# Optimization experiments

Measured on AMD Instinct MI355X. Metric: run time of the kernel, lower is better.

The kernel has to match this reference:

```python
import jax, jax.numpy as jnp
import numpy as np

B, C, H, W = 8, 512, 64, 128
K = 19          # num_classes
BH, BW = 2, 4   # bin_size
N = BH * BW     # bin_num
CI = C // 2     # feat_inner


def setup_inputs() -> dict:
    ks = jax.random.split(jax.random.key(0), 10)
    def nrm(k, shape, s=0.02):
        return jax.random.normal(k, shape, jnp.float32) * s
    return {
        "x": jax.random.normal(ks[0], (B, C, H, W), jnp.float32),
        "conv_cam_w": nrm(ks[1], (K, C)),
        "conv_cam_b": jnp.zeros((K,), jnp.float32),
        "gcn_w1": nrm(ks[2], (N, N), 0.1),
        "gcn_a": jnp.full((N,), 0.25, jnp.float32),
        "gcn_w2": nrm(ks[3], (C, C)),
        "fuse_w": nrm(ks[4], (1, N), 0.1),
        "fuse_b": jnp.zeros((1,), jnp.float32),
        "relu_a": jnp.full((1,), 0.25, jnp.float32),
        "q_w": nrm(ks[5], (CI, C)),
        "q_b": jnp.zeros((CI,), jnp.float32),
        "k_w": nrm(ks[6], (CI, C)),
        "k_b": jnp.zeros((CI,), jnp.float32),
        "v_w": nrm(ks[7], (CI, C)),
        "v_b": jnp.zeros((CI,), jnp.float32),
        "out_w": nrm(ks[8], (C, CI)),
        "bn_gamma": jnp.ones((C,), jnp.float32),
        "bn_beta": jnp.zeros((C,), jnp.float32),
        "out_a": jnp.full((C,), 0.25, jnp.float32),
    }


def _prelu(x, a):
    return jnp.maximum(x, 0) + a * jnp.minimum(x, 0)


def _split(t):
    # [b, cc, H, W] -> [b, N, rh*rw, cc]  (patch_split)
    b, cc = t.shape[0], t.shape[1]
    rh, rw = H // BH, W // BW
    t = t.reshape(b, cc, BH, rh, BW, rw).transpose(0, 2, 4, 3, 5, 1)
    return t.reshape(b, N, rh * rw, cc)


def _caam(x, conv_cam_w, conv_cam_b, gcn_w1, gcn_a, gcn_w2, fuse_w, fuse_b,
          relu_a, q_w, q_b, k_w, k_b, v_w, v_b, out_w, bn_gamma, bn_beta, out_a):
    b = x.shape[0]
    rh, rw = H // BH, W // BW
    # CAM (1x1 conv) + adaptive avg pool to bins + sigmoid
    cam = jnp.einsum('bchw,kc->bkhw', x, conv_cam_w) + conv_cam_b[None, :, None, None]
    cls_score = jax.nn.sigmoid(cam.reshape(b, K, BH, rh, BW, rw).mean((3, 5)))  # [b,K,BH,BW]
    cam_p = _split(cam)   # [b,N,P,K]
    x_p = _split(x)       # [b,N,P,C]
    bin_conf = cls_score.reshape(b, K, N).transpose(0, 2, 1)[..., None]  # [b,N,K,1]
    pix_conf = jax.nn.softmax(cam_p, axis=2)
    local = jnp.einsum('bnpk,bnpc->bnkc', pix_conf, x_p) * bin_conf  # [b,N,K,C]
    # GCN: conv1 over bin dim, PReLU(residual), Linear over channels
    t = jnp.einsum('nm,bmkc->bnkc', gcn_w1, local)
    t = _prelu(t + local, gcn_a[None, :, None, None])
    local = jnp.einsum('bnkc,dc->bnkd', t, gcn_w2)
    # fuse bins -> single global descriptor, PReLU(1)
    glob = jnp.einsum('on,bnkc->bokc', fuse_w, local) + fuse_b[None, :, None, None]  # [b,1,K,C]
    glob = _prelu(glob[:, 0], relu_a[0])  # [b,K,C]
    # QKV attention over bins (key/value over K class slots)
    q = jnp.einsum('bnpc,ic->bnpi', x_p, q_w) + q_b       # [b,N,P,CI]
    key = jnp.einsum('bnkc,ic->bnki', local, k_w) + k_b   # [b,N,K,CI]
    val = jnp.einsum('bkc,ic->bki', glob, v_w) + v_b      # [b,K,CI] (shared across bins)
    aff = jax.nn.softmax(jnp.einsum('bnpi,bnki->bnpk', q, key), axis=-1)
    out = jnp.einsum('bnpk,bki->bnpi', aff, val)          # [b,N,P,CI]
    # patch_recover -> [b,CI,H,W]
    out = out.reshape(b, BH, BW, rh, rw, CI).transpose(0, 5, 1, 3, 2, 4).reshape(b, CI, H, W)
    # conv_out: 1x1 conv (no bias) + BatchNorm2d (batch stats) + PReLU(C)
    y = jnp.einsum('bihw,ci->bchw', out, out_w)
    mu = y.mean((0, 2, 3), keepdims=True)
    var = y.var((0, 2, 3), keepdims=True)
    y = (y - mu) * jax.lax.rsqrt(var + 1e-5)
    y = y * bn_gamma[None, :, None, None] + bn_beta[None, :, None, None]
    y = _prelu(y, out_a[None, :, None, None])
    return x + y


def reference(x, conv_cam_w, conv_cam_b, gcn_w1, gcn_a, gcn_w2, fuse_w, fuse_b,
              relu_a, q_w, q_b, k_w, k_b, v_w, v_b, out_w, bn_gamma, bn_beta, out_a):
    return _caam(x, conv_cam_w, conv_cam_b, gcn_w1, gcn_a, gcn_w2, fuse_w, fuse_b,
                 relu_a, q_w, q_b, k_w, k_b, v_w, v_b, out_w, bn_gamma, bn_beta, out_a)
```

## Files before the change

### kernel.cpp

```cpp
#include <hip/hip_runtime.h>
#include <cstdint>
#include <cstddef>

#define B_ 8
#define C_ 512
#define H_ 64
#define W_ 128
#define HW_ 8192
#define K_ 19
#define N_ 8
#define P_ 1024
#define CI_ 256

typedef unsigned short u16;
typedef unsigned int u32;
typedef __attribute__((ext_vector_type(8))) short bf16x8;
typedef __attribute__((ext_vector_type(4))) float f32x4;

__device__ __forceinline__ u16 f2bf(float f) {
  u32 u = __float_as_uint(f);
  u32 r = (u + 0x7FFFu + ((u >> 16) & 1u)) >> 16;
  return (u16)r;
}
__device__ __forceinline__ float bf2f(u16 h) {
  return __uint_as_float(((u32)h) << 16);
}

__device__ __forceinline__ void gload16(const u16* g, u16* l) {
  __builtin_amdgcn_global_load_lds(
      (const __attribute__((address_space(1))) unsigned int*)g,
      (__attribute__((address_space(3))) unsigned int*)l, 16, 0, 0);
}

__device__ __forceinline__ void stage128(const u16* __restrict__ src, size_t ld, int k0,
                                         u16* lds, int wave, int lane) {
  int rsub = lane >> 3;
  int swz = ((lane & 7) ^ rsub) << 3;
#pragma unroll
  for (int i = 0; i < 4; i++) {
    int rowbase = wave * 8 + i * 32;
    gload16(src + (size_t)(rowbase + rsub) * ld + k0 + swz, lds + rowbase * 64);
  }
}
__device__ __forceinline__ void stage32(const u16* __restrict__ src, size_t ld, int k0,
                                        u16* lds, int wave, int lane) {
  int rsub = lane >> 3;
  int swz = ((lane & 7) ^ rsub) << 3;
  int rowbase = wave * 8;
  gload16(src + (size_t)(rowbase + rsub) * ld + k0 + swz, lds + rowbase * 64);
}
__device__ __forceinline__ bf16x8 frag(const u16* lds, int row, int qbyte) {
  return *(const bf16x8*)((const char*)lds + row * 128 + (qbyte ^ ((row & 7) << 4)));
}

__device__ __forceinline__ float blockSum256(float v, float* red4) {
#pragma unroll
  for (int o = 32; o > 0; o >>= 1) v += __shfl_down(v, o, 64);
  __syncthreads();
  if ((threadIdx.x & 63) == 0) red4[threadIdx.x >> 6] = v;
  __syncthreads();
  return red4[0] + red4[1] + red4[2] + red4[3];
}

__device__ __forceinline__ float blockMax256(float v, float* red4) {
#pragma unroll
  for (int o = 32; o > 0; o >>= 1) v = fmaxf(v, __shfl_down(v, o, 64));
  __syncthreads();
  if ((threadIdx.x & 63) == 0) red4[threadIdx.x >> 6] = v;
  __syncthreads();
  return fmaxf(fmaxf(red4[0], red4[1]), fmaxf(red4[2], red4[3]));
}

__device__ __forceinline__ void cvt4(const float* __restrict__ s, u16* __restrict__ d, int i) {
  float4 v = *(const float4*)&s[(size_t)i * 4];
  ushort4 o;
  o.x = f2bf(v.x); o.y = f2bf(v.y); o.z = f2bf(v.z); o.w = f2bf(v.w);
  *(ushort4*)&d[(size_t)i * 4] = o;
}

__global__ __launch_bounds__(256) void xpose_prep_kernel(const float* __restrict__ x,
                                                         u16* __restrict__ xt,
                                                         const float* __restrict__ qw,
                                                         const float* __restrict__ ow,
                                                         const float* __restrict__ kw,
                                                         const float* __restrict__ gw2,
                                                         const float* __restrict__ camw,
                                                         u16* __restrict__ qwbf,
                                                         u16* __restrict__ owbf,
                                                         u16* __restrict__ kwbf,
                                                         u16* __restrict__ gw2bf,
                                                         u16* __restrict__ camwbf,
                                                         float* __restrict__ sums,
                                                         float* __restrict__ tpad) {
  __shared__ float tile[64][65];
  int bid = blockIdx.x;
  int tid = threadIdx.x;
  if (bid >= 8192) {
    int pb = bid - 8192;
    if (pb < 128) {
      cvt4(qw, qwbf, pb * 256 + tid);
    } else if (pb < 256) {
      cvt4(ow, owbf, (pb - 128) * 256 + tid);
    } else if (pb < 384) {
      cvt4(kw, kwbf, (pb - 256) * 256 + tid);
    } else if (pb < 640) {
      cvt4(gw2, gw2bf, (pb - 384) * 256 + tid);
    } else if (pb < 656) {
      int i = (pb - 640) * 256 + tid;
      if (i * 4 < K_ * C_) {
        cvt4(camw, camwbf, i);
      } else {
        ushort4 z; z.x = 0; z.y = 0; z.z = 0; z.w = 0;
        *(ushort4*)&camwbf[(size_t)i * 4] = z;
      }
    } else if (pb == 656) {
      float4 z; z.x = 0.f; z.y = 0.f; z.z = 0.f; z.w = 0.f;
      *(float4*)&sums[tid * 4] = z;
    } else {
      int i = (pb - 657) * 256 + tid;
      float4 z; z.x = 0.f; z.y = 0.f; z.z = 0.f; z.w = 0.f;
      *(float4*)&tpad[(size_t)i * 4] = z;
    }
    return;
  }
  int hw0 = (bid & 127) << 6;
  int c0 = ((bid >> 7) & 7) << 6;
  int b = bid >> 10;
  int r = tid >> 4;
  int col4 = (tid & 15) << 2;
  const float* xb = x + ((size_t)b * C_ + c0) * HW_ + hw0;
#pragma unroll
  for (int it = 0; it < 4; it++) {
    int rr = r + it * 16;
    float4 v = *(const float4*)&xb[(size_t)rr * HW_ + col4];
    tile[rr][col4 + 0] = v.x;
    tile[rr][col4 + 1] = v.y;
    tile[rr][col4 + 2] = v.z;
    tile[rr][col4 + 3] = v.w;
  }
  __syncthreads();
  u16* xo = xt + ((size_t)b * HW_ + hw0) * C_ + c0;
#pragma unroll
  for (int it = 0; it < 4; it++) {
    int hwr = r + it * 16;
    ushort4 o;
    o.x = f2bf(tile[col4 + 0][hwr]);
    o.y = f2bf(tile[col4 + 1][hwr]);
    o.z = f2bf(tile[col4 + 2][hwr]);
    o.w = f2bf(tile[col4 + 3][hwr]);
    *(ushort4*)&xo[(size_t)hwr * C_ + col4] = o;
  }
}

__global__ __launch_bounds__(256) void gemm_cam_kernel(const u16* __restrict__ A,
                                                       const u16* __restrict__ Bw,
                                                       const float* __restrict__ bias,
                                                       float* __restrict__ cam) {
  __shared__ __align__(16) u16 As[128 * 64];
  __shared__ __align__(16) u16 Bs[32 * 64];
  int b = blockIdx.y;
  int m0 = blockIdx.x * 128;
  int tid = threadIdx.x;
  int wave = tid >> 6, lane = tid & 63;
  int wm = wave * 32;
  int quad = lane >> 4, l16 = lane & 15;
  const u16* Ab = A + (size_t)b * HW_ * C_ + (size_t)m0 * C_;
  f32x4 acc[2][2] = {};
  for (int k0 = 0; k0 < C_; k0 += 64) {
    __syncthreads();
    stage128(Ab, C_, k0, As, wave, lane);
    stage32(Bw, C_, k0, Bs, wave, lane);
    __syncthreads();
#pragma unroll
    for (int kk = 0; kk < 2; kk++) {
      int qb_ = kk * 64 + quad * 16;
      bf16x8 af[2], bfv[2];
#pragma unroll
      for (int t = 0; t < 2; t++) {
        af[t] = frag(As, wm + t * 16 + l16, qb_);
        bfv[t] = frag(Bs, t * 16 + l16, qb_);
      }
#pragma unroll
      for (int tm = 0; tm < 2; tm++)
#pragma unroll
        for (int tn = 0; tn < 2; tn++)
          acc[tm][tn] = __builtin_amdgcn_mfma_f32_16x16x32_bf16(af[tm], bfv[tn], acc[tm][tn], 0, 0, 0);
    }
  }
  float* C = cam + (size_t)b * K_ * HW_;
#pragma unroll
  for (int tm = 0; tm < 2; tm++) {
    int mm = m0 + wm + tm * 16 + quad * 4;
#pragma unroll
    for (int tn = 0; tn < 2; tn++) {
      int nn = tn * 16 + l16;
      if (nn < K_) {
        float bv = bias[nn];
        f32x4 v = acc[tm][tn];
        v[0] += bv; v[1] += bv; v[2] += bv; v[3] += bv;
        *(f32x4*)&C[(size_t)nn * HW_ + mm] = v;
      }
    }
  }
}

__global__ __launch_bounds__(256) void softcls_kernel(const float* __restrict__ cam,
                                                      float* __restrict__ bconf,
                                                      float* __restrict__ pconf) {
  __shared__ float red4[4];
  int bid = blockIdx.x;
  int k = bid % 19;
  int n = (bid / 19) & 7;
  int b = bid / 152;
  int bh = n >> 2, bw = n & 3;
  const float* base = cam + ((size_t)b * K_ + k) * HW_ + (bh * 32) * W_ + bw * 32;
  float v[4];
  float s = 0.f, mx = -1e30f;
#pragma unroll
  for (int j = 0; j < 4; j++) {
    int p = threadIdx.x + j * 256;
    v[j] = base[(p >> 5) * W_ + (p & 31)];
    s += v[j];
    mx = fmaxf(mx, v[j]);
  }
  float tot = blockSum256(s, red4);
  if (threadIdx.x == 0) {
    float m = tot * (1.f / 1024.f);
    bconf[bid] = 1.f / (1.f + __expf(-m));
  }
  mx = blockMax256(mx, red4);
  float e[4];
  float se = 0.f;
#pragma unroll
  for (int j = 0; j < 4; j++) { e[j] = __expf(v[j] - mx); se += e[j]; }
  se = blockSum256(se, red4);
  float inv = 1.f / se;
  float* outp = pconf + (size_t)bid * P_;
#pragma unroll
  for (int j = 0; j < 4; j++) outp[threadIdx.x + j * 256] = e[j] * inv;
}

__global__ __launch_bounds__(256) void local_part_kernel(const u16* __restrict__ xt,
                                                         const float* __restrict__ pconf,
                                                         float* __restrict__ part) {
  __shared__ __align__(16) float pcl[19 * 256];
  int bid = blockIdx.x;
  int pq = bid & 3;
  int half = (bid >> 2) & 1;
  int n = (bid >> 3) & 7;
  int b = bid >> 6;
  int tid = threadIdx.x;
  int c = half * 256 + tid;
  int bh = n >> 2, bw = n & 3;
  const float* pcb = pconf + (size_t)((b * N_ + n) * K_) * P_ + pq * 256;
  for (int e = tid; e < 19 * 64; e += 256) {
    int k = e >> 6, q4 = e & 63;
    *(float4*)&pcl[k * 256 + q4 * 4] = *(const float4*)&pcb[(size_t)k * P_ + q4 * 4];
  }
  __syncthreads();
  float acc[K_];
#pragma unroll
  for (int k = 0; k < K_; k++) acc[k] = 0.f;
  const u16* xb = xt + (size_t)b * HW_ * C_ + c;
  for (int pl0 = 0; pl0 < 256; pl0 += 8) {
    float xv[8];
#pragma unroll
    for (int g = 0; g < 2; g++) {
      int p = pq * 256 + pl0 + g * 4;
      int hw = (bh * 32 + (p >> 5)) * W_ + bw * 32 + (p & 31);
      const u16* xr = xb + (size_t)hw * C_;
#pragma unroll
      for (int j = 0; j < 4; j++) xv[g * 4 + j] = bf2f(xr[(size_t)j * C_]);
    }
#pragma unroll
    for (int k = 0; k < K_; k++) {
      float4 p0 = *(const float4*)&pcl[k * 256 + pl0];
      float4 p1 = *(const float4*)&pcl[k * 256 + pl0 + 4];
      acc[k] += p0.x * xv[0] + p0.y * xv[1] + p0.z * xv[2] + p0.w * xv[3]
              + p1.x * xv[4] + p1.y * xv[5] + p1.z * xv[6] + p1.w * xv[7];
    }
  }
  int row = (b * N_ + n) * K_;
  float* pp = part + ((size_t)pq * 1216 + row) * C_ + c;
#pragma unroll
  for (int k = 0; k < K_; k++) pp[(size_t)k * C_] = acc[k];
}

__global__ __launch_bounds__(256) void t_kernel(const float* __restrict__ part,
                                                const float* __restrict__ bconf,
                                                const float* __restrict__ gw1,
                                                const float* __restrict__ ga,
                                                u16* __restrict__ tbuf) {
  __shared__ float gw1l[64];
  __shared__ float gal[8];
  __shared__ float bcl[8];
  int tid = threadIdx.x;
  int bid = blockIdx.x;
  int half = bid & 1;
  int rem = bid >> 1;
  int k = rem % 19;
  int b = rem / 19;
  if (tid < 64) gw1l[tid] = gw1[tid];
  if (tid < 8) {
    gal[tid] = ga[tid];
    bcl[tid] = bconf[(size_t)(b * 8 + tid) * 19 + k];
  }
  __syncthreads();
  int c = half * 256 + tid;
  float lm[8];
#pragma unroll
  for (int m = 0; m < 8; m++) {
    size_t off = ((size_t)(b * N_ + m) * K_ + k) * C_ + c;
    lm[m] = (part[off] + part[off + (size_t)1216 * 512] +
             part[off + (size_t)2 * 1216 * 512] + part[off + (size_t)3 * 1216 * 512]) * bcl[m];
  }
#pragma unroll
  for (int n = 0; n < 8; n++) {
    float v = lm[n];
#pragma unroll
    for (int m = 0; m < 8; m++) v += gw1l[n * 8 + m] * lm[m];
    float t = fmaxf(v, 0.f) + gal[n] * fminf(v, 0.f);
    tbuf[((size_t)((b * N_ + n) * K_ + k)) * C_ + c] = f2bf(t);
  }
}

template <int KDIM, int NDIM, bool BIAS>
__device__ __forceinline__ void gemm_small_body(int bidx,
                                                const u16* __restrict__ A,
                                                const u16* __restrict__ Bw,
                                                const float* __restrict__ bias,
                                                float* __restrict__ f32out,
                                                u16* __restrict__ bf16out,
                                                u16* As, u16* Bs) {
  constexpr int NT = NDIM / 128;
  int m0 = (bidx / NT) * 128;
  int n0 = (bidx % NT) * 128;
  int tid = threadIdx.x;
  int wave = tid >> 6, lane = tid & 63;
  int wm = (wave >> 1) * 64, wn = (wave & 1) * 64;
  int quad = lane >> 4, l16 = lane & 15;
  const u16* Ab = A + (size_t)m0 * KDIM;
  const u16* Bb = Bw + (size_t)n0 * KDIM;
  f32x4 acc[4][4] = {};
  for (int k0 = 0; k0 < KDIM; k0 += 64) {
    __syncthreads();
    stage128(Ab, KDIM, k0, As, wave, lane);
    stage128(Bb, KDIM, k0, Bs, wave, lane);
    __syncthreads();
#pragma unroll
    for (int kk = 0; kk < 2; kk++) {
      int qb_ = kk * 64 + quad * 16;
      bf16x8 af[4], bfv[4];
#pragma unroll
      for (int t = 0; t < 4; t++) {
        af[t] = frag(As, wm + t * 16 + l16, qb_);
        bfv[t] = frag(Bs, wn + t * 16 + l16, qb_);
      }
#pragma unroll
      for (int tm = 0; tm < 4; tm++)
#pragma unroll
        for (int tn = 0; tn < 4; tn++)
          acc[tm][tn] = __builtin_amdgcn_mfma_f32_16x16x32_bf16(af[tm], bfv[tn], acc[tm][tn], 0, 0, 0);
    }
  }
  float bv[4];
#pragma unroll
  for (int tn = 0; tn < 4; tn++)
    bv[tn] = BIAS ? bias[n0 + wn + tn * 16 + l16] : 0.f;
#pragma unroll
  for (int tm = 0; tm < 4; tm++) {
    int mm = m0 + wm + tm * 16 + quad * 4;
#pragma unroll
    for (int tn = 0; tn < 4; tn++) {
      int nn = n0 + wn + tn * 16 + l16;
#pragma unroll
      for (int reg = 0; reg < 4; reg++) {
        float v = acc[tm][tn][reg] + bv[tn];
        if (f32out) f32out[(size_t)(mm + reg) * NDIM + nn] = v;
        if (bf16out) bf16out[(size_t)(mm + reg) * NDIM + nn] = f2bf(v);
      }
    }
  }
}

template <int KDIM, int NDIM, bool BIAS>
__global__ __launch_bounds__(256) void gemm_small_kernel(const u16* __restrict__ A,
                                                         const u16* __restrict__ Bw,
                                                         const float* __restrict__ bias,
                                                         float* __restrict__ f32out,
                                                         u16* __restrict__ bf16out) {
  __shared__ __align__(16) u16 As[128 * 64];
  __shared__ __align__(16) u16 Bs[128 * 64];
  gemm_small_body<KDIM, NDIM, BIAS>(blockIdx.x, A, Bw, bias, f32out, bf16out, As, Bs);
}

__device__ __forceinline__ void glob_val_body(int bid,
                                              const float* __restrict__ locl2,
                                              const float* __restrict__ fw,
                                              const float* __restrict__ fb,
                                              const float* __restrict__ ra,
                                              const float* __restrict__ vw,
                                              const float* __restrict__ vb,
                                              float* __restrict__ valo,
                                              float* gl) {
  int k = bid % 19;
  int b = bid / 19;
  int tid = threadIdx.x;
  float fwr[8];
#pragma unroll
  for (int m = 0; m < 8; m++) fwr[m] = fw[m];
  float fbv = fb[0], rav = ra[0];
  const float* lb = locl2 + ((size_t)(b * N_) * K_ + k) * C_;
  for (int c = tid; c < C_; c += 256) {
    float v = fbv;
#pragma unroll
    for (int m = 0; m < 8; m++) v += fwr[m] * lb[(size_t)m * K_ * C_ + c];
    gl[c] = fmaxf(v, 0.f) + rav * fminf(v, 0.f);
  }
  __syncthreads();
  int i = tid;
  const float* wr = vw + (size_t)i * C_;
  float s = vb[i];
  for (int c4 = 0; c4 < C_; c4 += 4) {
    float4 wv = *(const float4*)&wr[c4];
    float4 tv = *(const float4*)&gl[c4];
    s += wv.x * tv.x + wv.y * tv.y + wv.z * tv.z + wv.w * tv.w;
  }
  valo[(size_t)bid * CI_ + i] = s;
}

__global__ __launch_bounds__(256) void small2_globval_kernel(const u16* __restrict__ A,
                                                             const u16* __restrict__ Bw,
                                                             const float* __restrict__ bias,
                                                             float* __restrict__ keyo,
                                                             const float* __restrict__ locl2,
                                                             const float* __restrict__ fw,
                                                             const float* __restrict__ fb,
                                                             const float* __restrict__ ra,
                                                             const float* __restrict__ vw,
                                                             const float* __restrict__ vb,
                                                             float* __restrict__ valo) {
  __shared__ __align__(16) u16 As[128 * 64];
  __shared__ __align__(16) u16 Bs[128 * 64];
  if (blockIdx.x < 20) {
    gemm_small_body<512, 256, true>(blockIdx.x, A, Bw, bias, keyo, nullptr, As, Bs);
  } else {
    glob_val_body(blockIdx.x - 20, locl2, fw, fb, ra, vw, vb, valo, (float*)As);
  }
}

template <int KDIM, int NDIM, bool TRANS_OUT, bool BIAS, bool OUTBF16, bool BNSTAT>
__global__ __launch_bounds__(256) void gemm_big_kernel(const u16* __restrict__ A,
                                                       const u16* __restrict__ Bw,
                                                       const float* __restrict__ bias,
                                                       void* __restrict__ Cout,
                                                       float* __restrict__ sums,
                                                       float* __restrict__ sumsq) {
  __shared__ __align__(16) u16 As[128 * 64];
  __shared__ __align__(16) u16 Bs[128 * 64];
  constexpr int NT = NDIM / 128;
  int b = blockIdx.y;
  int d = blockIdx.x;
  int xcd = d & 7;
  int j = d >> 3;
  int m0 = (xcd + 8 * (j / NT)) * 128;
  int n0 = (j % NT) * 128;
  int tid = threadIdx.x;
  int wave = tid >> 6, lane = tid & 63;
  int wm = (wave >> 1) * 64, wn = (wave & 1) * 64;
  int quad = lane >> 4, l16 = lane & 15;
  const u16* Ab = A + (size_t)b * 8192 * KDIM + (size_t)m0 * KDIM;
  const u16* Bb = Bw + (size_t)n0 * KDIM;
  f32x4 acc[4][4] = {};
  for (int k0 = 0; k0 < KDIM; k0 += 64) {
    __syncthreads();
    stage128(Ab, KDIM, k0, As, wave, lane);
    stage128(Bb, KDIM, k0, Bs, wave, lane);
    __syncthreads();
#pragma unroll
    for (int kk = 0; kk < 2; kk++) {
      int qb_ = kk * 64 + quad * 16;
      bf16x8 af[4], bfv[4];
#pragma unroll
      for (int t = 0; t < 4; t++) {
        af[t] = frag(As, wm + t * 16 + l16, qb_);
        bfv[t] = frag(Bs, wn + t * 16 + l16, qb_);
      }
#pragma unroll
      for (int tm = 0; tm < 4; tm++)
#pragma unroll
        for (int tn = 0; tn < 4; tn++)
          acc[tm][tn] = __builtin_amdgcn_mfma_f32_16x16x32_bf16(af[tm], bfv[tn], acc[tm][tn], 0, 0, 0);
    }
  }
  if constexpr (!TRANS_OUT) {
    float bv[4];
#pragma unroll
    for (int tn = 0; tn < 4; tn++)
      bv[tn] = BIAS ? bias[n0 + wn + tn * 16 + l16] : 0.f;
#pragma unroll
    for (int tm = 0; tm < 4; tm++) {
      int mm = m0 + wm + tm * 16 + quad * 4;
#pragma unroll
      for (int tn = 0; tn < 4; tn++) {
        int nn = n0 + wn + tn * 16 + l16;
        if constexpr (OUTBF16) {
          u16* C = (u16*)Cout + (size_t)b * 8192 * NDIM;
#pragma unroll
          for (int reg = 0; reg < 4; reg++)
            C[(size_t)(mm + reg) * NDIM + nn] = f2bf(acc[tm][tn][reg] + bv[tn]);
        } else {
          float* C = (float*)Cout + (size_t)b * 8192 * NDIM;
#pragma unroll
          for (int reg = 0; reg < 4; reg++)
            C[(size_t)(mm + reg) * NDIM + nn] = acc[tm][tn][reg] + bv[tn];
        }
      }
    }
  } else {
    float* C = (float*)Cout + (size_t)b * NDIM * 8192;
#pragma unroll
    for (int tm = 0; tm < 4; tm++) {
      int mm = m0 + wm + tm * 16 + quad * 4;
#pragma unroll
      for (int tn = 0; tn < 4; tn++) {
        int nn = n0 + wn + tn * 16 + l16;
        *(f32x4*)&C[(size_t)nn * 8192 + mm] = acc[tm][tn];
      }
    }
    if constexpr (BNSTAT) {
#pragma unroll
      for (int tn = 0; tn < 4; tn++) {
        int nn = n0 + wn + tn * 16 + l16;
        float s = 0.f, q = 0.f;
#pragma unroll
        for (int tm = 0; tm < 4; tm++)
#pragma unroll
          for (int reg = 0; reg < 4; reg++) {
            float v = acc[tm][tn][reg];
            s += v;
            q += v * v;
          }
        s += __shfl_xor(s, 16, 64); q += __shfl_xor(q, 16, 64);
        s += __shfl_xor(s, 32, 64); q += __shfl_xor(q, 32, 64);
        if (quad == 0) {
          atomicAdd(&sums[nn], s);
          atomicAdd(&sumsq[nn], q);
        }
      }
    }
  }
}

__global__ __launch_bounds__(256) void attn2_kernel(const u16* __restrict__ q,
                                                    const float* __restrict__ keyo,
                                                    const float* __restrict__ valo,
                                                    u16* __restrict__ obuf) {
  __shared__ float keyl[19 * 256];
  __shared__ float vall[19 * 256];
  __shared__ float aff[128 * 20];
  int bid = blockIdx.x;
  int rg = bid & 7;
  int n = (bid >> 3) & 7;
  int b = bid >> 6;
  int bh = n >> 2, bw = n & 3;
  int tid = threadIdx.x;
  const float* ksrc = keyo + (size_t)((b * 8 + n) * 19) * 256;
  for (int e = tid; e < 19 * 256; e += 256) keyl[e] = ksrc[e];
  __syncthreads();
  if (tid < 128) {
    int r = rg * 4 + (tid >> 5);
    int wc = tid & 31;
    int hw = (bh * 32 + r) * W_ + bw * 32 + wc;
    const u16* qr = q + ((size_t)b * HW_ + hw) * 256;
    float acc[19];
#pragma unroll
    for (int k = 0; k < 19; k++) acc[k] = 0.f;
    for (int i0 = 0; i0 < 256; i0 += 8) {
      uint4 v = *(const uint4*)&qr[i0];
      float f0 = __uint_as_float((v.x & 0xFFFFu) << 16);
      float f1 = __uint_as_float(v.x & 0xFFFF0000u);
      float f2 = __uint_as_float((v.y & 0xFFFFu) << 16);
      float f3 = __uint_as_float(v.y & 0xFFFF0000u);
      float f4 = __uint_as_float((v.z & 0xFFFFu) << 16);
      float f5 = __uint_as_float(v.z & 0xFFFF0000u);
      float f6 = __uint_as_float((v.w & 0xFFFFu) << 16);
      float f7 = __uint_as_float(v.w & 0xFFFF0000u);
#pragma unroll
      for (int k = 0; k < 19; k++) {
        const float* kr = &keyl[k * 256 + i0];
        acc[k] += f0 * kr[0] + f1 * kr[1] + f2 * kr[2] + f3 * kr[3] +
                  f4 * kr[4] + f5 * kr[5] + f6 * kr[6] + f7 * kr[7];
      }
    }
    float mx = -1e30f;
#pragma unroll
    for (int k = 0; k < 19; k++) mx = fmaxf(mx, acc[k]);
    float se = 0.f;
#pragma unroll
    for (int k = 0; k < 19; k++) { acc[k] = __expf(acc[k] - mx); se += acc[k]; }
    float inv = 1.f / se;
#pragma unroll
    for (int k = 0; k < 19; k++) aff[tid * 20 + k] = acc[k] * inv;
  } else {
    const float* vsrc = valo + (size_t)b * 19 * 256;
    for (int e = tid - 128; e < 19 * 256; e += 128) vall[e] = vsrc[e];
  }
  __syncthreads();
  int px = tid & 127;
  int ih = (tid >> 7) * 128;
  int r3 = rg * 4 + (px >> 5);
  int wc3 = px & 31;
  int hw3 = (bh * 32 + r3) * W_ + bw * 32 + wc3;
  float av[19];
#pragma unroll
  for (int k = 0; k < 19; k++) av[k] = aff[px * 20 + k];
  u16* ob = obuf + ((size_t)b * HW_ + hw3) * 256 + ih;
  for (int i0 = 0; i0 < 128; i0 += 16) {
    float o16[16];
#pragma unroll
    for (int j = 0; j < 16; j++) o16[j] = 0.f;
#pragma unroll
    for (int k = 0; k < 19; k++) {
      float a = av[k];
      const float* vr = &vall[k * 256 + ih + i0];
#pragma unroll
      for (int j = 0; j < 16; j++) o16[j] += a * vr[j];
    }
    uint4 w0, w1;
    w0.x = (u32)f2bf(o16[0]) | ((u32)f2bf(o16[1]) << 16);
    w0.y = (u32)f2bf(o16[2]) | ((u32)f2bf(o16[3]) << 16);
    w0.z = (u32)f2bf(o16[4]) | ((u32)f2bf(o16[5]) << 16);
    w0.w = (u32)f2bf(o16[6]) | ((u32)f2bf(o16[7]) << 16);
    w1.x = (u32)f2bf(o16[8]) | ((u32)f2bf(o16[9]) << 16);
    w1.y = (u32)f2bf(o16[10]) | ((u32)f2bf(o16[11]) << 16);
    w1.z = (u32)f2bf(o16[12]) | ((u32)f2bf(o16[13]) << 16);
    w1.w = (u32)f2bf(o16[14]) | ((u32)f2bf(o16[15]) << 16);
    *(uint4*)&ob[i0] = w0;
    *(uint4*)&ob[i0 + 8] = w1;
  }
}

__global__ __launch_bounds__(256) void final_kernel(const float* __restrict__ x,
                                                    const float* __restrict__ sums,
                                                    const float* __restrict__ sumsq,
                                                    const float* __restrict__ gamma,
                                                    const float* __restrict__ beta,
                                                    const float* __restrict__ oa,
                                                    float* __restrict__ out) {
  size_t base = (size_t)blockIdx.x * 4096 + threadIdx.x * 4;
  int c = (int)((base >> 13) & 511);
  const float inv_cnt = 1.f / 65536.f;
  float mu = sums[c] * inv_cnt;
  float var = sumsq[c] * inv_cnt - mu * mu;
  float iv = rsqrtf(var + 1e-5f);
  float sc = gamma[c] * iv;
  float sh = beta[c] - mu * sc;
  float a = oa[c];
#pragma unroll
  for (int jj = 0; jj < 4; jj++) {
    size_t idx = base + (size_t)jj * 1024;
    float4 y = *(float4*)&out[idx];
    float4 xv = *(const float4*)&x[idx];
    float4 r;
    float t;
    t = y.x * sc + sh; r.x = xv.x + fmaxf(t, 0.f) + a * fminf(t, 0.f);
    t = y.y * sc + sh; r.y = xv.y + fmaxf(t, 0.f) + a * fminf(t, 0.f);
    t = y.z * sc + sh; r.z = xv.z + fmaxf(t, 0.f) + a * fminf(t, 0.f);
    t = y.w * sc + sh; r.w = xv.w + fmaxf(t, 0.f) + a * fminf(t, 0.f);
    *(float4*)&out[idx] = r;
  }
}

extern "C" void kernel_launch(void* const* d_in, const int* in_sizes, int n_in,
                              void* d_out, int out_size, void* d_ws, size_t ws_size,
                              hipStream_t stream) {
  const float* x     = (const float*)d_in[0];
  const float* camw  = (const float*)d_in[1];
  const float* camb  = (const float*)d_in[2];
  const float* gw1   = (const float*)d_in[3];
  const float* ga    = (const float*)d_in[4];
  const float* gw2   = (const float*)d_in[5];
  const float* fw    = (const float*)d_in[6];
  const float* fb    = (const float*)d_in[7];
  const float* ra    = (const float*)d_in[8];
  const float* qw    = (const float*)d_in[9];
  const float* qb    = (const float*)d_in[10];
  const float* kw    = (const float*)d_in[11];
  const float* kb    = (const float*)d_in[12];
  const float* vw    = (const float*)d_in[13];
  const float* vb    = (const float*)d_in[14];
  const float* ow    = (const float*)d_in[15];
  const float* gamma = (const float*)d_in[16];
  const float* beta  = (const float*)d_in[17];
  const float* oa    = (const float*)d_in[18];
  float* out = (float*)d_out;
  float* ws = (float*)d_ws;

  float* cam    = ws;
  float* bconf  = cam + 1245184;
  float* pconf  = bconf + 2048;
  float* locl   = pconf + 1245184;
  float* locl2f = locl + 622592;
  float* keyo   = locl2f + 655360;
  float* valo   = keyo + 327680;
  float* sums   = valo + 38912;
  float* sumsq  = sums + 512;
  float* scale  = sumsq + 512;
  float* shift  = scale + 512;
  u16* qwbf   = (u16*)(shift + 512);
  u16* owbf   = qwbf + 131072;
  u16* kwbf   = owbf + 131072;
  u16* gw2bf  = kwbf + 131072;
  u16* camwbf = gw2bf + 262144;
  u16* tbuf   = camwbf + 16384;
  u16* l2bf   = tbuf + 655360;
  u16* xt     = l2bf + 655360;
  u16* obuf   = xt;
  u16* qbuf   = xt + 33554432;
  float* part = (float*)qbuf;

  xpose_prep_kernel<<<8865, 256, 0, stream>>>(x, xt, qw, ow, kw, gw2, camw,
                                              qwbf, owbf, kwbf, gw2bf, camwbf,
                                              sums, (float*)(tbuf + 1216 * 512));
  gemm_cam_kernel<<<dim3(64, 8), 256, 0, stream>>>(xt, camwbf, camb, cam);
  softcls_kernel<<<1216, 256, 0, stream>>>(cam, bconf, pconf);
  local_part_kernel<<<512, 256, 0, stream>>>(xt, pconf, part);
  t_kernel<<<304, 256, 0, stream>>>(part, bconf, gw1, ga, tbuf);
  gemm_small_kernel<512, 512, false>
      <<<40, 256, 0, stream>>>(tbuf, gw2bf, nullptr, locl2f, l2bf);
  small2_globval_kernel<<<172, 256, 0, stream>>>(l2bf, kwbf, kb, keyo,
                                                 locl2f, fw, fb, ra, vw, vb, valo);
  gemm_big_kernel<512, 256, false, true, true, false>
      <<<dim3(128, 8), 256, 0, stream>>>(xt, qwbf, qb, qbuf, nullptr, nullptr);
  attn2_kernel<<<512, 256, 0, stream>>>(qbuf, keyo, valo, obuf);
  gemm_big_kernel<256, 512, true, false, false, true>
      <<<dim3(256, 8), 256, 0, stream>>>(obuf, owbf, nullptr, out, sums, sumsq);
  final_kernel<<<8192, 256, 0, stream>>>(x, sums, sumsq, gamma, beta, oa, out);
}
```

Before: 549.3 us.

## Fold query and output projections into low-rank key/value products

Reassociates the attention: each bin's keys are pre-multiplied by the query weights (qw^T·key, giving a 512x19 matrix per bin plus a bias term). The values are pre-multiplied by the output conv weights, giving a 19x512 matrix per batch. Affinities then come from a thin GEMM of x against 19 columns, and the output is rebuilt as aff·vo inside the final kernel, with BN statistics computed from the affinities. This removes the two big 8192x512x256 GEMMs and the bf16 intermediate q/o buffers. The cost is recomputing y in a scalar loop in the final kernel with strided per-channel stores, plus a small serial weight-fold kernel.

```diff
diff --git a/kernel.cpp b/kernel.cpp
--- a/kernel.cpp
+++ b/kernel.cpp
@@ -80,13 +80,9 @@
 
 __global__ __launch_bounds__(256) void xpose_prep_kernel(const float* __restrict__ x,
                                                          u16* __restrict__ xt,
-                                                         const float* __restrict__ qw,
-                                                         const float* __restrict__ ow,
                                                          const float* __restrict__ kw,
                                                          const float* __restrict__ gw2,
                                                          const float* __restrict__ camw,
-                                                         u16* __restrict__ qwbf,
-                                                         u16* __restrict__ owbf,
                                                          u16* __restrict__ kwbf,
                                                          u16* __restrict__ gw2bf,
                                                          u16* __restrict__ camwbf,
@@ -98,26 +94,22 @@
   if (bid >= 8192) {
     int pb = bid - 8192;
     if (pb < 128) {
-      cvt4(qw, qwbf, pb * 256 + tid);
-    } else if (pb < 256) {
-      cvt4(ow, owbf, (pb - 128) * 256 + tid);
+      cvt4(kw, kwbf, pb * 256 + tid);
     } else if (pb < 384) {
-      cvt4(kw, kwbf, (pb - 256) * 256 + tid);
-    } else if (pb < 640) {
-      cvt4(gw2, gw2bf, (pb - 384) * 256 + tid);
-    } else if (pb < 656) {
-      int i = (pb - 640) * 256 + tid;
+      cvt4(gw2, gw2bf, (pb - 128) * 256 + tid);
+    } else if (pb < 400) {
+      int i = (pb - 384) * 256 + tid;
       if (i * 4 < K_ * C_) {
         cvt4(camw, camwbf, i);
       } else {
         ushort4 z; z.x = 0; z.y = 0; z.z = 0; z.w = 0;
         *(ushort4*)&camwbf[(size_t)i * 4] = z;
       }
-    } else if (pb == 656) {
+    } else if (pb == 400) {
       float4 z; z.x = 0.f; z.y = 0.f; z.z = 0.f; z.w = 0.f;
       *(float4*)&sums[tid * 4] = z;
     } else {
-      int i = (pb - 657) * 256 + tid;
+      int i = (pb - 401) * 256 + tid;
       float4 z; z.x = 0.f; z.y = 0.f; z.z = 0.f; z.w = 0.f;
       *(float4*)&tpad[(size_t)i * 4] = z;
     }
@@ -449,226 +441,217 @@
   }
 }
 
-template <int KDIM, int NDIM, bool TRANS_OUT, bool BIAS, bool OUTBF16, bool BNSTAT>
-__global__ __launch_bounds__(256) void gemm_big_kernel(const u16* __restrict__ A,
-                                                       const u16* __restrict__ Bw,
-                                                       const float* __restrict__ bias,
-                                                       void* __restrict__ Cout,
-                                                       float* __restrict__ sums,
-                                                       float* __restrict__ sumsq) {
+__global__ __launch_bounds__(256) void qk2vo_kernel(const float* __restrict__ keyo,
+                                                    const float* __restrict__ qw,
+                                                    const float* __restrict__ qb,
+                                                    const float* __restrict__ valo,
+                                                    const float* __restrict__ ow,
+                                                    u16* __restrict__ qk2bf,
+                                                    float* __restrict__ sbias,
+                                                    float* __restrict__ vo) {
+  __shared__ float kl[19 * 256];
+  int bid = blockIdx.x, tid = threadIdx.x;
+  if (bid < 64) {
+    const float* ks = keyo + (size_t)bid * 19 * 256;
+    for (int e = tid; e < 19 * 256; e += 256) kl[e] = ks[e];
+    __syncthreads();
+    if (tid < 19) {
+      float s = 0.f;
+      for (int i = 0; i < 256; i++) s += qb[i] * kl[tid * 256 + i];
+      sbias[(size_t)bid * 19 + tid] = s;
+    }
+    float a0[19], a1[19];
+#pragma unroll
+    for (int k = 0; k < 19; k++) { a0[k] = 0.f; a1[k] = 0.f; }
+    for (int i = 0; i < 256; i++) {
+      float q0 = qw[(size_t)i * 512 + tid];
+      float q1 = qw[(size_t)i * 512 + 256 + tid];
+#pragma unroll
+      for (int k = 0; k < 19; k++) {
+        float kv = kl[k * 256 + i];
+        a0[k] += q0 * kv;
+        a1[k] += q1 * kv;
+      }
+    }
+    u16* qo = qk2bf + (size_t)bid * 32 * 512;
+#pragma unroll
+    for (int k = 0; k < 19; k++) {
+      qo[k * 512 + tid] = f2bf(a0[k]);
+      qo[k * 512 + 256 + tid] = f2bf(a1[k]);
+    }
+  } else {
+    int b = bid - 64;
+    const float* vs = valo + (size_t)b * 19 * 256;
+    for (int e = tid; e < 19 * 256; e += 256) kl[e] = vs[e];
+    __syncthreads();
+    float a0[19], a1[19];
+#pragma unroll
+    for (int k = 0; k < 19; k++) { a0[k] = 0.f; a1[k] = 0.f; }
+    for (int i = 0; i < 256; i++) {
+      float w0 = ow[(size_t)tid * 256 + i];
+      float w1 = ow[(size_t)(tid + 256) * 256 + i];
+#pragma unroll
+      for (int k = 0; k < 19; k++) {
+        float kv = kl[k * 256 + i];
+        a0[k] += w0 * kv;
+        a1[k] += w1 * kv;
+      }
+    }
+    float* vob = vo + (size_t)b * 19 * 512;
+#pragma unroll
+    for (int k = 0; k < 19; k++) {
+      vob[k * 512 + tid] = a0[k];
+      vob[k * 512 + 256 + tid] = a1[k];
+    }
+  }
+}
+
+__global__ __launch_bounds__(256) void attn3_kernel(const u16* __restrict__ xt,
+                                                    const u16* __restrict__ qk2bf,
+                                                    const float* __restrict__ sbias,
+                                                    const float* __restrict__ vo,
+                                                    float* __restrict__ aff,
+                                                    float* __restrict__ sums,
+                                                    float* __restrict__ sumsq) {
   __shared__ __align__(16) u16 As[128 * 64];
-  __shared__ __align__(16) u16 Bs[128 * 64];
-  constexpr int NT = NDIM / 128;
-  int b = blockIdx.y;
-  int d = blockIdx.x;
-  int xcd = d & 7;
-  int j = d >> 3;
-  int m0 = (xcd + 8 * (j / NT)) * 128;
-  int n0 = (j % NT) * 128;
+  __shared__ __align__(16) u16 Bs[32 * 64];
+  __shared__ __align__(16) float aff_l[128][24];
+  int bid = blockIdx.x;
+  int mt = bid & 7, n = (bid >> 3) & 7, b = bid >> 6;
+  int bh = n >> 2, bw = n & 3;
   int tid = threadIdx.x;
   int wave = tid >> 6, lane = tid & 63;
-  int wm = (wave >> 1) * 64, wn = (wave & 1) * 64;
+  int wm = wave * 32;
   int quad = lane >> 4, l16 = lane & 15;
-  const u16* Ab = A + (size_t)b * 8192 * KDIM + (size_t)m0 * KDIM;
-  const u16* Bb = Bw + (size_t)n0 * KDIM;
-  f32x4 acc[4][4] = {};
-  for (int k0 = 0; k0 < KDIM; k0 += 64) {
+  int hwbase = bh * 4096 + bw * 32 + mt * 512;
+  const u16* Ab = xt + ((size_t)b * HW_ + hwbase) * C_;
+  const u16* Bb = qk2bf + (size_t)(b * 8 + n) * 32 * 512;
+  f32x4 acc[2][2] = {};
+  int rsub = lane >> 3;
+  int swz = ((lane & 7) ^ rsub) << 3;
+  for (int k0 = 0; k0 < C_; k0 += 64) {
     __syncthreads();
-    stage128(Ab, KDIM, k0, As, wave, lane);
-    stage128(Bb, KDIM, k0, Bs, wave, lane);
+#pragma unroll
+    for (int i = 0; i < 4; i++) {
+      int rb = wave * 8 + i * 32;
+      int r = rb + rsub;
+      gload16(Ab + (size_t)((r >> 5) * 128 + (r & 31)) * C_ + k0 + swz, As + rb * 64);
+    }
+    stage32(Bb, 512, k0, Bs, wave, lane);
     __syncthreads();
 #pragma unroll
     for (int kk = 0; kk < 2; kk++) {
       int qb_ = kk * 64 + quad * 16;
-      bf16x8 af[4], bfv[4];
-#pragma unroll
-      for (int t = 0; t < 4; t++) {
-        af[t] = frag(As, wm + t * 16 + l16, qb_);
-        bfv[t] = frag(Bs, wn + t * 16 + l16, qb_);
+      bf16x8 af2[2], bfv[2];
+#pragma unroll
+      for (int t = 0; t < 2; t++) {
+        af2[t] = frag(As, wm + t * 16 + l16, qb_);
+        bfv[t] = frag(Bs, t * 16 + l16, qb_);
       }
 #pragma unroll
-      for (int tm = 0; tm < 4; tm++)
-#pragma unroll
-        for (int tn = 0; tn < 4; tn++)
-          acc[tm][tn] = __builtin_amdgcn_mfma_f32_16x16x32_bf16(af[tm], bfv[tn], acc[tm][tn], 0, 0, 0);
-    }
-  }
-  if constexpr (!TRANS_OUT) {
-    float bv[4];
-#pragma unroll
-    for (int tn = 0; tn < 4; tn++)
-      bv[tn] = BIAS ? bias[n0 + wn + tn * 16 + l16] : 0.f;
-#pragma unroll
-    for (int tm = 0; tm < 4; tm++) {
-      int mm = m0 + wm + tm * 16 + quad * 4;
-#pragma unroll
-      for (int tn = 0; tn < 4; tn++) {
-        int nn = n0 + wn + tn * 16 + l16;
-        if constexpr (OUTBF16) {
-          u16* C = (u16*)Cout + (size_t)b * 8192 * NDIM;
-#pragma unroll
-          for (int reg = 0; reg < 4; reg++)
-            C[(size_t)(mm + reg) * NDIM + nn] = f2bf(acc[tm][tn][reg] + bv[tn]);
-        } else {
-          float* C = (float*)Cout + (size_t)b * 8192 * NDIM;
-#pragma unroll
-          for (int reg = 0; reg < 4; reg++)
-            C[(size_t)(mm + reg) * NDIM + nn] = acc[tm][tn][reg] + bv[tn];
-        }
-      }
-    }
-  } else {
-    float* C = (float*)Cout + (size_t)b * NDIM * 8192;
-#pragma unroll
-    for (int tm = 0; tm < 4; tm++) {
-      int mm = m0 + wm + tm * 16 + quad * 4;
-#pragma unroll
-      for (int tn = 0; tn < 4; tn++) {
-        int nn = n0 + wn + tn * 16 + l16;
-        *(f32x4*)&C[(size_t)nn * 8192 + mm] = acc[tm][tn];
-      }
-    }
-    if constexpr (BNSTAT) {
-#pragma unroll
-      for (int tn = 0; tn < 4; tn++) {
-        int nn = n0 + wn + tn * 16 + l16;
-        float s = 0.f, q = 0.f;
-#pragma unroll
-        for (int tm = 0; tm < 4; tm++)
-#pragma unroll
-          for (int reg = 0; reg < 4; reg++) {
-            float v = acc[tm][tn][reg];
-            s += v;
-            q += v * v;
-          }
-        s += __shfl_xor(s, 16, 64); q += __shfl_xor(q, 16, 64);
-        s += __shfl_xor(s, 32, 64); q += __shfl_xor(q, 32, 64);
-        if (quad == 0) {
-          atomicAdd(&sums[nn], s);
-          atomicAdd(&sumsq[nn], q);
-        }
-      }
-    }
-  }
-}
-
-__global__ __launch_bounds__(256) void attn2_kernel(const u16* __restrict__ q,
-                                                    const float* __restrict__ keyo,
-                                                    const float* __restrict__ valo,
-                                                    u16* __restrict__ obuf) {
-  __shared__ float keyl[19 * 256];
-  __shared__ float vall[19 * 256];
-  __shared__ float aff[128 * 20];
-  int bid = blockIdx.x;
-  int rg = bid & 7;
-  int n = (bid >> 3) & 7;
-  int b = bid >> 6;
-  int bh = n >> 2, bw = n & 3;
-  int tid = threadIdx.x;
-  const float* ksrc = keyo + (size_t)((b * 8 + n) * 19) * 256;
-  for (int e = tid; e < 19 * 256; e += 256) keyl[e] = ksrc[e];
-  __syncthreads();
-  if (tid < 128) {
-    int r = rg * 4 + (tid >> 5);
-    int wc = tid & 31;
-    int hw = (bh * 32 + r) * W_ + bw * 32 + wc;
-    const u16* qr = q + ((size_t)b * HW_ + hw) * 256;
-    float acc[19];
-#pragma unroll
-    for (int k = 0; k < 19; k++) acc[k] = 0.f;
-    for (int i0 = 0; i0 < 256; i0 += 8) {
-      uint4 v = *(const uint4*)&qr[i0];
-      float f0 = __uint_as_float((v.x & 0xFFFFu) << 16);
-      float f1 = __uint_as_float(v.x & 0xFFFF0000u);
-      float f2 = __uint_as_float((v.y & 0xFFFFu) << 16);
-      float f3 = __uint_as_float(v.y & 0xFFFF0000u);
-      float f4 = __uint_as_float((v.z & 0xFFFFu) << 16);
-      float f5 = __uint_as_float(v.z & 0xFFFF0000u);
-      float f6 = __uint_as_float((v.w & 0xFFFFu) << 16);
-      float f7 = __uint_as_float(v.w & 0xFFFF0000u);
-#pragma unroll
-      for (int k = 0; k < 19; k++) {
-        const float* kr = &keyl[k * 256 + i0];
-        acc[k] += f0 * kr[0] + f1 * kr[1] + f2 * kr[2] + f3 * kr[3] +
-                  f4 * kr[4] + f5 * kr[5] + f6 * kr[6] + f7 * kr[7];
-      }
-    }
-    float mx = -1e30f;
-#pragma unroll
-    for (int k = 0; k < 19; k++) mx = fmaxf(mx, acc[k]);
-    float se = 0.f;
-#pragma unroll
-    for (int k = 0; k < 19; k++) { acc[k] = __expf(acc[k] - mx); se += acc[k]; }
-    float inv = 1.f / se;
-#pragma unroll
-    for (int k = 0; k < 19; k++) aff[tid * 20 + k] = acc[k] * inv;
-  } else {
-    const float* vsrc = valo + (size_t)b * 19 * 256;
-    for (int e = tid - 128; e < 19 * 256; e += 128) vall[e] = vsrc[e];
-  }
-  __syncthreads();
-  int px = tid & 127;
-  int ih = (tid >> 7) * 128;
-  int r3 = rg * 4 + (px >> 5);
-  int wc3 = px & 31;
-  int hw3 = (bh * 32 + r3) * W_ + bw * 32 + wc3;
-  float av[19];
-#pragma unroll
-  for (int k = 0; k < 19; k++) av[k] = aff[px * 20 + k];
-  u16* ob = obuf + ((size_t)b * HW_ + hw3) * 256 + ih;
-  for (int i0 = 0; i0 < 128; i0 += 16) {
-    float o16[16];
-#pragma unroll
-    for (int j = 0; j < 16; j++) o16[j] = 0.f;
-#pragma unroll
-    for (int k = 0; k < 19; k++) {
-      float a = av[k];
-      const float* vr = &vall[k * 256 + ih + i0];
-#pragma unroll
-      for (int j = 0; j < 16; j++) o16[j] += a * vr[j];
-    }
-    uint4 w0, w1;
-    w0.x = (u32)f2bf(o16[0]) | ((u32)f2bf(o16[1]) << 16);
-    w0.y = (u32)f2bf(o16[2]) | ((u32)f2bf(o16[3]) << 16);
-    w0.z = (u32)f2bf(o16[4]) | ((u32)f2bf(o16[5]) << 16);
-    w0.w = (u32)f2bf(o16[6]) | ((u32)f2bf(o16[7]) << 16);
-    w1.x = (u32)f2bf(o16[8]) | ((u32)f2bf(o16[9]) << 16);
-    w1.y = (u32)f2bf(o16[10]) | ((u32)f2bf(o16[11]) << 16);
-    w1.z = (u32)f2bf(o16[12]) | ((u32)f2bf(o16[13]) << 16);
-    w1.w = (u32)f2bf(o16[14]) | ((u32)f2bf(o16[15]) << 16);
-    *(uint4*)&ob[i0] = w0;
-    *(uint4*)&ob[i0 + 8] = w1;
-  }
+      for (int tm = 0; tm < 2; tm++)
+#pragma unroll
+        for (int tn = 0; tn < 2; tn++)
+          acc[tm][tn] = __builtin_amdgcn_mfma_f32_16x16x32_bf16(af2[tm], bfv[tn], acc[tm][tn], 0, 0, 0);
+    }
+  }
+  const float* sb = sbias + (size_t)(b * 8 + n) * 19;
+  float sb0 = sb[l16];
+  float sb1 = (l16 < 3) ? sb[16 + l16] : 0.f;
+#pragma unroll
+  for (int tm = 0; tm < 2; tm++)
+#pragma unroll
+    for (int reg = 0; reg < 4; reg++) {
+      float v0 = acc[tm][0][reg] + sb0;
+      float v1 = (l16 < 3) ? (acc[tm][1][reg] + sb1) : -1e30f;
+      float mx = fmaxf(v0, v1);
+#pragma unroll
+      for (int o = 8; o > 0; o >>= 1) mx = fmaxf(mx, __shfl_xor(mx, o, 16));
+      float e0 = __expf(v0 - mx);
+      float e1 = (l16 < 3) ? __expf(v1 - mx) : 0.f;
+      float s = e0 + e1;
+#pragma unroll
+      for (int o = 8; o > 0; o >>= 1) s += __shfl_xor(s, o, 16);
+      float inv = 1.f / s;
+      int rl = wm + tm * 16 + quad * 4 + reg;
+      aff_l[rl][l16] = e0 * inv;
+      if (l16 < 3) aff_l[rl][16 + l16] = e1 * inv;
+    }
+  __syncthreads();
+  float* ab = aff + ((size_t)(b * 8 + n) * 19) * 1024 + mt * 128;
+  for (int e = tid; e < 19 * 128; e += 256) {
+    int k = e >> 7, px = e & 127;
+    ab[(size_t)k * 1024 + px] = aff_l[px][k];
+  }
+  const float* vob = vo + (size_t)b * 19 * 512;
+  float v0r[19], v1r[19];
+#pragma unroll
+  for (int k = 0; k < 19; k++) {
+    v0r[k] = vob[k * 512 + tid];
+    v1r[k] = vob[k * 512 + 256 + tid];
+  }
+  float s0 = 0.f, q0 = 0.f, s1 = 0.f, q1 = 0.f;
+  for (int px = 0; px < 128; px++) {
+    const float4* ar4 = (const float4*)aff_l[px];
+    float4 a0 = ar4[0], a1 = ar4[1], a2 = ar4[2], a3 = ar4[3], a4 = ar4[4];
+    float y0 = a0.x * v0r[0] + a0.y * v0r[1] + a0.z * v0r[2] + a0.w * v0r[3]
+             + a1.x * v0r[4] + a1.y * v0r[5] + a1.z * v0r[6] + a1.w * v0r[7]
+             + a2.x * v0r[8] + a2.y * v0r[9] + a2.z * v0r[10] + a2.w * v0r[11]
+             + a3.x * v0r[12] + a3.y * v0r[13] + a3.z * v0r[14] + a3.w * v0r[15]
+             + a4.x * v0r[16] + a4.y * v0r[17] + a4.z * v0r[18];
+    float y1 = a0.x * v1r[0] + a0.y * v1r[1] + a0.z * v1r[2] + a0.w * v1r[3]
+             + a1.x * v1r[4] + a1.y * v1r[5] + a1.z * v1r[6] + a1.w * v1r[7]
+             + a2.x * v1r[8] + a2.y * v1r[9] + a2.z * v1r[10] + a2.w * v1r[11]
+             + a3.x * v1r[12] + a3.y * v1r[13] + a3.z * v1r[14] + a3.w * v1r[15]
+             + a4.x * v1r[16] + a4.y * v1r[17] + a4.z * v1r[18];
+    s0 += y0; q0 += y0 * y0;
+    s1 += y1; q1 += y1 * y1;
+  }
+  atomicAdd(&sums[tid], s0);
+  atomicAdd(&sumsq[tid], q0);
+  atomicAdd(&sums[256 + tid], s1);
+  atomicAdd(&sumsq[256 + tid], q1);
 }
 
 __global__ __launch_bounds__(256) void final_kernel(const float* __restrict__ x,
+                                                    const float* __restrict__ aff,
+                                                    const float* __restrict__ vo,
                                                     const float* __restrict__ sums,
                                                     const float* __restrict__ sumsq,
                                                     const float* __restrict__ gamma,
                                                     const float* __restrict__ beta,
                                                     const float* __restrict__ oa,
                                                     float* __restrict__ out) {
-  size_t base = (size_t)blockIdx.x * 4096 + threadIdx.x * 4;
-  int c = (int)((base >> 13) & 511);
+  int bid = blockIdx.x;
+  int chunk = bid & 63, b = bid >> 6;
+  int tid = threadIdx.x;
+  int pxl = tid & 127;
+  int chalf = tid >> 7;
+  int hw = chunk * 128 + pxl;
+  int h = hw >> 7, w = hw & 127;
+  int n = (h >> 5) * 4 + (w >> 5);
+  int p = ((h & 31) << 5) + (w & 31);
+  const float* ab = aff + ((size_t)(b * 8 + n) * 19) * 1024 + p;
+  float af[19];
+#pragma unroll
+  for (int k = 0; k < 19; k++) af[k] = ab[(size_t)k * 1024];
+  const float* vob = vo + (size_t)b * 19 * 512;
   const float inv_cnt = 1.f / 65536.f;
-  float mu = sums[c] * inv_cnt;
-  float var = sumsq[c] * inv_cnt - mu * mu;
-  float iv = rsqrtf(var + 1e-5f);
-  float sc = gamma[c] * iv;
-  float sh = beta[c] - mu * sc;
-  float a = oa[c];
-#pragma unroll
-  for (int jj = 0; jj < 4; jj++) {
-    size_t idx = base + (size_t)jj * 1024;
-    float4 y = *(float4*)&out[idx];
-    float4 xv = *(const float4*)&x[idx];
-    float4 r;
-    float t;
-    t = y.x * sc + sh; r.x = xv.x + fmaxf(t, 0.f) + a * fminf(t, 0.f);
-    t = y.y * sc + sh; r.y = xv.y + fmaxf(t, 0.f) + a * fminf(t, 0.f);
-    t = y.z * sc + sh; r.z = xv.z + fmaxf(t, 0.f) + a * fminf(t, 0.f);
-    t = y.w * sc + sh; r.w = xv.w + fmaxf(t, 0.f) + a * fminf(t, 0.f);
-    *(float4*)&out[idx] = r;
+  size_t base = (size_t)b * C_ * HW_ + hw;
+  int c0 = chalf * 256;
+  for (int c = c0; c < c0 + 256; c++) {
+    float y = 0.f;
+#pragma unroll
+    for (int k = 0; k < 19; k++) y += af[k] * vob[k * 512 + c];
+    float mu = sums[c] * inv_cnt;
+    float var = sumsq[c] * inv_cnt - mu * mu;
+    float iv = rsqrtf(var + 1e-5f);
+    float sc = gamma[c] * iv;
+    float sh = beta[c] - mu * sc;
+    float t = y * sc + sh;
+    float pr = fmaxf(t, 0.f) + oa[c] * fminf(t, 0.f);
+    size_t o = base + (size_t)c * HW_;
+    out[o] = x[o] + pr;
   }
 }
 
@@ -700,28 +683,25 @@
   float* cam    = ws;
   float* bconf  = cam + 1245184;
   float* pconf  = bconf + 2048;
-  float* locl   = pconf + 1245184;
-  float* locl2f = locl + 622592;
+  float* aff    = pconf + 1245184;
+  float* locl2f = aff + 1245184;
   float* keyo   = locl2f + 655360;
   float* valo   = keyo + 327680;
   float* sums   = valo + 38912;
   float* sumsq  = sums + 512;
-  float* scale  = sumsq + 512;
-  float* shift  = scale + 512;
-  u16* qwbf   = (u16*)(shift + 512);
-  u16* owbf   = qwbf + 131072;
-  u16* kwbf   = owbf + 131072;
+  float* sbias  = sumsq + 512;
+  float* vo     = sbias + 1216;
+  float* part   = vo + 77824;
+  u16* kwbf   = (u16*)(part + 2490368);
   u16* gw2bf  = kwbf + 131072;
   u16* camwbf = gw2bf + 262144;
   u16* tbuf   = camwbf + 16384;
   u16* l2bf   = tbuf + 655360;
-  u16* xt     = l2bf + 655360;
-  u16* obuf   = xt;
-  u16* qbuf   = xt + 33554432;
-  float* part = (float*)qbuf;
-
-  xpose_prep_kernel<<<8865, 256, 0, stream>>>(x, xt, qw, ow, kw, gw2, camw,
-                                              qwbf, owbf, kwbf, gw2bf, camwbf,
+  u16* qk2bf  = l2bf + 655360;
+  u16* xt     = qk2bf + 1048576;
+
+  xpose_prep_kernel<<<8609, 256, 0, stream>>>(x, xt, kw, gw2, camw,
+                                              kwbf, gw2bf, camwbf,
                                               sums, (float*)(tbuf + 1216 * 512));
   gemm_cam_kernel<<<dim3(64, 8), 256, 0, stream>>>(xt, camwbf, camb, cam);
   softcls_kernel<<<1216, 256, 0, stream>>>(cam, bconf, pconf);
@@ -731,10 +711,7 @@
       <<<40, 256, 0, stream>>>(tbuf, gw2bf, nullptr, locl2f, l2bf);
   small2_globval_kernel<<<172, 256, 0, stream>>>(l2bf, kwbf, kb, keyo,
                                                  locl2f, fw, fb, ra, vw, vb, valo);
-  gemm_big_kernel<512, 256, false, true, true, false>
-      <<<dim3(128, 8), 256, 0, stream>>>(xt, qwbf, qb, qbuf, nullptr, nullptr);
-  attn2_kernel<<<512, 256, 0, stream>>>(qbuf, keyo, valo, obuf);
-  gemm_big_kernel<256, 512, true, false, false, true>
-      <<<dim3(256, 8), 256, 0, stream>>>(obuf, owbf, nullptr, out, sums, sumsq);
-  final_kernel<<<8192, 256, 0, stream>>>(x, sums, sumsq, gamma, beta, oa, out);
-}
+  qk2vo_kernel<<<72, 256, 0, stream>>>(keyo, qw, qb, valo, ow, qk2bf, sbias, vo);
+  attn3_kernel<<<512, 256, 0, stream>>>(xt, qk2bf, sbias, vo, aff, sums, sumsq);
+  final_kernel<<<512, 256, 0, stream>>>(x, aff, vo, sums, sumsq, gamma, beta, oa, out);
+}
```

Measured after the change: 667.4 us. 21.5% more time.
